# Kernel optimization log

Measured on AMD Instinct MI355X. Metric: run time of the kernel, lower is better.

## Reference

```python
import jax, jax.numpy as jnp
import numpy as np

K = 16          # self.nn_size
BALL2 = 0.2     # ball_size * 2, compared against squared L2 dists (faiss convention)

def _knn(q, db, k):
    # squared L2 pairwise distances (B,N,M) via ||q||^2 + ||db||^2 - 2 q.db
    d2 = (jnp.sum(q * q, -1)[..., None]
          + jnp.sum(db * db, -1)[..., None, :]
          - 2.0 * jnp.einsum('bnc,bmc->bnm', q, db))
    neg_d, idx = jax.lax.top_k(-d2, k)   # k smallest distances
    return -neg_d, idx                    # (B,N,K), (B,N,K)

def _cond_numbers(grouped, nball, B, N, C):
    # center by masked-ball mean, then singular values of (K,C) groups
    center = jnp.sum(grouped, axis=2, keepdims=True) / nball[..., None]
    centered = (grouped - center).reshape(-1, K, C)
    S = jnp.linalg.svd(centered, compute_uv=False)   # descending, (B*N, min(K,C))
    return (S[:, 0] / (S[:, -1] + S[:, 0])).reshape(B, N)

def setup_inputs() -> dict:
    key = jax.random.key(0)
    k1, k2 = jax.random.split(key)
    ref_points = jax.random.uniform(k1, (2, 8192, 3), dtype=jnp.float32)
    points = jax.random.uniform(k2, (2, 8192, 3), dtype=jnp.float32)
    return {"ref_points": ref_points, "points": points}

def reference(ref_points, points):
    B, N, C = ref_points.shape
    dist, idx = _knn(ref_points, ref_points, K)
    mask = dist < BALL2                                  # (B,N,K)
    nball = jnp.sum(mask.astype(ref_points.dtype), -1, keepdims=True)  # (B,N,1)

    gather = jax.vmap(lambda p, i: p[i])                 # (N,C),(N,K)->(N,K,C)
    grouped_ref = gather(ref_points, idx)                # (B,N,K,C)
    grouped_ref = jnp.where(mask[..., None], grouped_ref, 0.0)  # masked_fill_ (in-place, kept)
    ref_cond = _cond_numbers(grouped_ref, nball, B, N, C)

    grouped = gather(points, idx)                        # (B,N,K,C)
    # NOTE: original calls masked_fill (non-inplace) and DISCARDS the result -> no masking here
    cond = _cond_numbers(grouped, nball, B, N, C)

    # metric: MSE with mean reduction
    return jnp.mean((cond - ref_cond) ** 2)
```

## Files before the change

kernel.cpp:

```cpp
#include <hip/hip_runtime.h>

#define NPTS   8192
#define KNN    16
#define G      10
#define NCELLS 1000
#define CAP    32
#define CELLSZ 0.1f
#define BALL2f 0.2f
#define TRUNCM 0xFFFFE000u
#define IDXM   0x1FFFu
#define NBLK   256
#define FLTMAX 3.402823466e+38f

#define WS_ACC   0
#define WS_DONE  8
#define WS_CNT   16
#define WS_RSORT 8224
#define WS_ZERO  8216

__device__ __forceinline__ int clampg(int v) { return v < 0 ? 0 : (v > G - 1 ? G - 1 : v); }

__global__ __launch_bounds__(256) void bin_kernel(
        const float* __restrict__ ref, int* __restrict__ gcnt,
        float4* __restrict__ rs) {
    int t = blockIdx.x * 256 + threadIdx.x;
    if (t >= 2 * NPTS) return;
    int b = t >> 13, i = t & (NPTS - 1);
    const float* rb = ref + (size_t)b * NPTS * 3 + 3 * (size_t)i;
    float x = rb[0], y = rb[1], z = rb[2];
    int c = (clampg((int)(z * (float)G)) * G + clampg((int)(y * (float)G))) * G
          + clampg((int)(x * (float)G));
    int slot = atomicAdd(&gcnt[b * NCELLS + c], 1);
    if (slot < CAP)
        rs[(size_t)b * NCELLS * CAP + c * CAP + slot] =
            make_float4(x, y, z, __uint_as_float((unsigned)i));
}

__device__ __forceinline__ double cond3(double xx, double xy, double xz,
                                        double yy, double yz, double zz) {
    double q  = (xx + yy + zz) * (1.0 / 3.0);
    double a  = xx - q, b = yy - q, c = zz - q;
    double p1 = xy * xy + xz * xz + yz * yz;
    double p2 = a * a + b * b + c * c + 2.0 * p1;
    if (p2 <= 0.0) return 0.5;
    double p   = sqrt(p2 * (1.0 / 6.0));
    double inv = 1.0 / p;
    double b00 = a * inv, b11 = b * inv, b22 = c * inv;
    double b01 = xy * inv, b02 = xz * inv, b12 = yz * inv;
    double detB = b00 * (b11 * b22 - b12 * b12)
                - b01 * (b01 * b22 - b12 * b02)
                + b02 * (b01 * b12 - b11 * b02);
    double r = 0.5 * detB;
    r = fmin(1.0, fmax(-1.0, r));
    double phi = acos(r) * (1.0 / 3.0);
    double l0 = q + 2.0 * p * cos(phi);
    double l2 = q + 2.0 * p * cos(phi + 2.0943951023931953);
    double s0 = sqrt(fmax(l0, 0.0));
    double s2 = sqrt(fmax(l2, 0.0));
    return s0 / (s0 + s2);
}

__global__ __launch_bounds__(1024) void cond_knn_kernel(
        const float* __restrict__ ref, const float* __restrict__ pts,
        const float4* __restrict__ rs, const int* __restrict__ gcnt,
        double* __restrict__ acc, int* __restrict__ done,
        float* __restrict__ out) {
    __shared__ unsigned sld[8][64][17];
    __shared__ int scnt[1024];
    __shared__ int ss[1025];
    __shared__ int wsum[16];
    __shared__ unsigned cutp[64];
    __shared__ unsigned char doneA[64];
    __shared__ int flagS;

    const int tid  = threadIdx.x;
    const int w    = tid >> 6;
    const int lane = tid & 63;
    const int b     = blockIdx.x >> 7;
    const int qbase = (blockIdx.x & 127) << 6;
    const float4* rs4 = rs + (size_t)b * NCELLS * CAP;

    int myc = 0;
    if (tid < NCELLS) { myc = gcnt[b * NCELLS + tid]; myc = myc > CAP ? CAP : myc; }
    scnt[tid] = myc;
    int v = myc;
    #pragma unroll
    for (int off = 1; off < 64; off <<= 1) {
        int u = __shfl_up(v, off, 64);
        if (lane >= off) v += u;
    }
    if (lane == 63) wsum[w] = v;
    __syncthreads();
    if (tid == 0) {
        int run = 0;
        for (int i2 = 0; i2 < 16; ++i2) { int tv = wsum[i2]; wsum[i2] = run; run += tv; }
    }
    __syncthreads();
    ss[tid + 1] = v + wsum[w];
    if (tid == 0) ss[0] = 0;
    __syncthreads();

    const int spos = qbase + lane;
    int lo = 0;
    #pragma unroll
    for (int stp = 512; stp >= 1; stp >>= 1) {
        int nlo = lo + stp;
        if (ss[nlo] <= spos) lo = nlo;
    }
    const int qc = lo;
    float4 Q = rs4[qc * CAP + (spos - ss[qc])];
    const float qx = Q.x, qy = Q.y, qz = Q.z;
    const int cx = clampg((int)(qx * (float)G));
    const int cy = clampg((int)(qy * (float)G));
    const int cz = clampg((int)(qz * (float)G));

    unsigned bq[KNN];
    #pragma unroll
    for (int k = 0; k < KNN; ++k) bq[k] = 0xFFFFFFFFu;

    auto scanRange = [&](int base, int s0, int s1, unsigned cutv) {
        for (int t2 = s0; t2 < s1; ++t2) {
            float4 P = rs4[base + t2];
            float dx = qx - P.x, dy = qy - P.y, dz = qz - P.z;
            float d = fmaf(dx, dx, fmaf(dy, dy, dz * dz));
            unsigned vk = (__float_as_uint(d) & TRUNCM) | __float_as_uint(P.w);
            unsigned cv = cutv < bq[15] ? cutv : bq[15];
            if (vk < cv) {
                bq[15] = vk;
                #pragma unroll
                for (int kk = 15; kk >= 1; --kk) {
                    unsigned l2 = min(bq[kk - 1], bq[kk]);
                    unsigned h2 = max(bq[kk - 1], bq[kk]);
                    bq[kk - 1] = l2; bq[kk] = h2;
                }
            }
        }
    };

    auto mergeToW0 = [&]() {
        #pragma unroll
        for (int rnd = 0; rnd < 4; ++rnd) {
            int s = 1 << rnd;
            int slot = w >> (rnd + 1);
            __syncthreads();
            if ((w & (2 * s - 1)) == s) {
                #pragma unroll
                for (int k = 0; k < KNN; ++k) sld[slot][lane][k] = bq[k];
            }
            __syncthreads();
            if ((w & (2 * s - 1)) == 0) {
                #pragma unroll
                for (int k = 0; k < KNN; ++k) {
                    unsigned vk = sld[slot][lane][k];
                    if (vk < bq[15]) {
                        bq[15] = vk;
                        #pragma unroll
                        for (int kk = 15; kk >= 1; --kk) {
                            unsigned l2 = min(bq[kk - 1], bq[kk]);
                            unsigned h2 = max(bq[kk - 1], bq[kk]);
                            bq[kk - 1] = l2; bq[kk] = h2;
                        }
                    }
                }
            }
        }
    };

    {
        int counter = 0;
        #pragma unroll
        for (int dz = -1; dz <= 1; ++dz)
        #pragma unroll
        for (int dy = -1; dy <= 1; ++dy)
        #pragma unroll
        for (int dx = -1; dx <= 1; ++dx) {
            #pragma unroll
            for (int h = 0; h < 2; ++h) {
                int cc = counter++;
                if ((cc & 15) != w) continue;
                int nx = cx + dx, ny = cy + dy, nz = cz + dz;
                if ((unsigned)nx > (unsigned)(G - 1) || (unsigned)ny > (unsigned)(G - 1) ||
                    (unsigned)nz > (unsigned)(G - 1)) continue;
                int cell = (nz * G + ny) * G + nx;
                int cnt = scnt[cell];
                int mid = cnt >> 1;
                if (h == 0) scanRange(cell * CAP, 0, mid, 0xFFFFFFFFu);
                else        scanRange(cell * CAP, mid, cnt, 0xFFFFFFFFu);
            }
        }
    }
    mergeToW0();

    int r_done = 1;
    while (true) {
        if (tid == 0) flagS = 0;
        __syncthreads();
        if (w == 0) {
            float mx = FLTMAX;
            if (cx - r_done > 0)     mx = fminf(mx, qx - (float)(cx - r_done) * CELLSZ);
            if (cx + r_done < G - 1) mx = fminf(mx, (float)(cx + r_done + 1) * CELLSZ - qx);
            if (cy - r_done > 0)     mx = fminf(mx, qy - (float)(cy - r_done) * CELLSZ);
            if (cy + r_done < G - 1) mx = fminf(mx, (float)(cy + r_done + 1) * CELLSZ - qy);
            if (cz - r_done > 0)     mx = fminf(mx, qz - (float)(cz - r_done) * CELLSZ);
            if (cz + r_done < G - 1) mx = fminf(mx, (float)(cz + r_done + 1) * CELLSZ - qz);
            float d16t = __uint_as_float(bq[15] & TRUNCM);
            bool dn = d16t <= mx * mx * 0.998f;
            cutp[lane]  = bq[15];
            doneA[lane] = dn ? 1 : 0;
            bool anyn = __any(!dn);
            if (anyn && lane == 0) flagS = 1;
        }
        __syncthreads();
        if (!flagS || r_done >= G) break;
        int r = r_done + 1;
        if (w != 0) {
            #pragma unroll
            for (int k = 0; k < KNN; ++k) bq[k] = 0xFFFFFFFFu;
        }
        unsigned cut = cutp[lane];
        float cutub = __uint_as_float(cut | IDXM);
        bool active = !doneA[lane];
        int counter = 0;
        for (int dz = -r; dz <= r; ++dz)
        for (int dy = -r; dy <= r; ++dy)
        for (int dx = -r; dx <= r; ++dx) {
            int adx = dx < 0 ? -dx : dx, ady = dy < 0 ? -dy : dy, adz = dz < 0 ? -dz : dz;
            int m = adx > ady ? adx : ady; m = m > adz ? m : adz;
            if (m != r) continue;
            int cc = counter++;
            if ((cc & 15) != w) continue;
            if (!active) continue;
            int nx = cx + dx, ny = cy + dy, nz = cz + dz;
            if ((unsigned)nx > (unsigned)(G - 1) || (unsigned)ny > (unsigned)(G - 1) ||
                (unsigned)nz > (unsigned)(G - 1)) continue;
            float ex0 = (float)nx * CELLSZ;
            float ey0 = (float)ny * CELLSZ;
            float ez0 = (float)nz * CELLSZ;
            float ddx = fmaxf(0.f, fmaxf(ex0 - qx, qx - ex0 - CELLSZ));
            float ddy = fmaxf(0.f, fmaxf(ey0 - qy, qy - ey0 - CELLSZ));
            float ddz = fmaxf(0.f, fmaxf(ez0 - qz, qz - ez0 - CELLSZ));
            float d2min = fmaf(ddx, ddx, fmaf(ddy, ddy, ddz * ddz));
            if (d2min > cutub) continue;
            int cell = (nz * G + ny) * G + nx;
            scanRange(cell * CAP, 0, scnt[cell], cut);
        }
        mergeToW0();
        r_done = r;
    }

    if (w != 0) return;

    const float* refb = ref + (size_t)b * NPTS * 3;
    const float* ptsb = pts + (size_t)b * NPTS * 3;
    float rx[KNN], ry[KNN], rz[KNN], px[KNN], py[KNN], pz[KNN];
    int mbits = 0;
    float sRx = 0.f, sRy = 0.f, sRz = 0.f, sPx = 0.f, sPy = 0.f, sPz = 0.f;
    #pragma unroll
    for (int k = 0; k < KNN; ++k) {
        int i = (int)(bq[k] & IDXM);
        float du = __uint_as_float(bq[k] & TRUNCM);
        rx[k] = refb[3 * i]; ry[k] = refb[3 * i + 1]; rz[k] = refb[3 * i + 2];
        px[k] = ptsb[3 * i]; py[k] = ptsb[3 * i + 1]; pz[k] = ptsb[3 * i + 2];
        if (du < BALL2f) {
            mbits |= (1 << k);
            sRx += rx[k]; sRy += ry[k]; sRz += rz[k];
        }
        sPx += px[k]; sPy += py[k]; sPz += pz[k];
    }
    int nb = __popc(mbits);
    double inb = 1.0 / (double)nb;
    double cRx = (double)sRx * inb, cRy = (double)sRy * inb, cRz = (double)sRz * inb;
    double cPx = (double)sPx * inb, cPy = (double)sPy * inb, cPz = (double)sPz * inb;

    double Rxx = 0, Rxy = 0, Rxz = 0, Ryy = 0, Ryz = 0, Rzz = 0;
    double Pxx = 0, Pxy = 0, Pxz = 0, Pyy = 0, Pyz = 0, Pzz = 0;
    #pragma unroll
    for (int k = 0; k < KNN; ++k) {
        bool m = (mbits >> k) & 1;
        double ax = (m ? (double)rx[k] : 0.0) - cRx;
        double ay = (m ? (double)ry[k] : 0.0) - cRy;
        double az = (m ? (double)rz[k] : 0.0) - cRz;
        Rxx += ax * ax; Rxy += ax * ay; Rxz += ax * az;
        Ryy += ay * ay; Ryz += ay * az; Rzz += az * az;
        double bx = (double)px[k] - cPx;
        double by = (double)py[k] - cPy;
        double bz = (double)pz[k] - cPz;
        Pxx += bx * bx; Pxy += bx * by; Pxz += bx * bz;
        Pyy += by * by; Pyz += by * bz; Pzz += bz * bz;
    }
    double condR = cond3(Rxx, Rxy, Rxz, Ryy, Ryz, Rzz);
    double condP = cond3(Pxx, Pxy, Pxz, Pyy, Pyz, Pzz);
    double t = condP - condR;
    t = t * t;

    #pragma unroll
    for (int off = 32; off > 0; off >>= 1) t += __shfl_down(t, off);
    if (lane == 0) {
        atomicAdd(acc, t);
        __threadfence();
        int prev = atomicAdd(done, 1);
        if (prev == NBLK - 1) {
            __threadfence();
            double total = atomicAdd(acc, 0.0);
            out[0] = (float)(total * (1.0 / 16384.0));
        }
    }
}

extern "C" void kernel_launch(void* const* d_in, const int* in_sizes, int n_in,
                              void* d_out, int out_size, void* d_ws, size_t ws_size,
                              hipStream_t stream) {
    const float* ref = (const float*)d_in[0];
    const float* pts = (const float*)d_in[1];
    char* ws = (char*)d_ws;
    double* acc   = (double*)(ws + WS_ACC);
    int* done     = (int*)(ws + WS_DONE);
    int* gcnt     = (int*)(ws + WS_CNT);
    float4* rsort = (float4*)(ws + WS_RSORT);

    hipMemsetAsync(ws, 0, WS_ZERO, stream);
    hipLaunchKernelGGL(bin_kernel,      dim3(64),   dim3(256),  0, stream, ref, gcnt, rsort);
    hipLaunchKernelGGL(cond_knn_kernel, dim3(NBLK), dim3(1024), 0, stream,
                       ref, pts, rsort, gcnt, acc, done, (float*)d_out);
}
```

Baseline: 105.4 us.

## Fuse memset, binning and kNN into one cooperative kernel; bitonic merge

Replaces the memset, bin kernel and kNN/cond kernel with a single cooperative launch. Zeroing and binning run inside it, separated by grid-wide syncs. The change also unrolls the candidate scan by four with an early min-reject check, and replaces the per-element insertion merge across waves with a bitonic merge of two sorted 16-lists. The aim is to remove two launch and memset overheads and cut merge cost, at the price of two grid barriers and cooperative-launch constraints.

```diff
diff --git a/kernel.cpp b/kernel.cpp
--- a/kernel.cpp
+++ b/kernel.cpp
@@ -1,4 +1,7 @@
 #include <hip/hip_runtime.h>
+#include <hip/hip_cooperative_groups.h>
+
+namespace cg = cooperative_groups;
 
 #define NPTS   8192
 #define KNN    16
@@ -16,25 +19,8 @@
 #define WS_DONE  8
 #define WS_CNT   16
 #define WS_RSORT 8224
-#define WS_ZERO  8216
 
 __device__ __forceinline__ int clampg(int v) { return v < 0 ? 0 : (v > G - 1 ? G - 1 : v); }
-
-__global__ __launch_bounds__(256) void bin_kernel(
-        const float* __restrict__ ref, int* __restrict__ gcnt,
-        float4* __restrict__ rs) {
-    int t = blockIdx.x * 256 + threadIdx.x;
-    if (t >= 2 * NPTS) return;
-    int b = t >> 13, i = t & (NPTS - 1);
-    const float* rb = ref + (size_t)b * NPTS * 3 + 3 * (size_t)i;
-    float x = rb[0], y = rb[1], z = rb[2];
-    int c = (clampg((int)(z * (float)G)) * G + clampg((int)(y * (float)G))) * G
-          + clampg((int)(x * (float)G));
-    int slot = atomicAdd(&gcnt[b * NCELLS + c], 1);
-    if (slot < CAP)
-        rs[(size_t)b * NCELLS * CAP + c * CAP + slot] =
-            make_float4(x, y, z, __uint_as_float((unsigned)i));
-}
 
 __device__ __forceinline__ double cond3(double xx, double xy, double xz,
                                         double yy, double yz, double zz) {
@@ -60,9 +46,9 @@
     return s0 / (s0 + s2);
 }
 
-__global__ __launch_bounds__(1024) void cond_knn_kernel(
+__global__ __launch_bounds__(1024) void fused_kernel(
         const float* __restrict__ ref, const float* __restrict__ pts,
-        const float4* __restrict__ rs, const int* __restrict__ gcnt,
+        int* __restrict__ gcnt, float4* __restrict__ rs,
         double* __restrict__ acc, int* __restrict__ done,
         float* __restrict__ out) {
     __shared__ unsigned sld[8][64][17];
@@ -76,8 +62,34 @@
     const int tid  = threadIdx.x;
     const int w    = tid >> 6;
     const int lane = tid & 63;
-    const int b     = blockIdx.x >> 7;
-    const int qbase = (blockIdx.x & 127) << 6;
+    const int blk  = blockIdx.x;
+
+    {
+        int z = blk * 8 + tid;
+        if (tid < 8 && z < 2 * NCELLS) gcnt[z] = 0;
+        if (blk == 0 && tid == 0) { acc[0] = 0.0; done[0] = 0; }
+    }
+    __threadfence();
+    cg::this_grid().sync();
+
+    if (tid < 64) {
+        int i = blk * 64 + tid;
+        int bb = i >> 13, ii = i & (NPTS - 1);
+        const float* rb = ref + (size_t)bb * NPTS * 3 + 3 * (size_t)ii;
+        float x = rb[0], y = rb[1], z = rb[2];
+        int c = (clampg((int)(z * (float)G)) * G + clampg((int)(y * (float)G))) * G
+              + clampg((int)(x * (float)G));
+        int slot = atomicAdd(&gcnt[bb * NCELLS + c], 1);
+        if (slot < CAP)
+            rs[(size_t)bb * NCELLS * CAP + c * CAP + slot] =
+                make_float4(x, y, z, __uint_as_float((unsigned)ii));
+    }
+    __threadfence();
+    cg::this_grid().sync();
+    __threadfence();
+
+    const int b     = blk >> 7;
+    const int qbase = (blk & 127) << 6;
     const float4* rs4 = rs + (size_t)b * NCELLS * CAP;
 
     int myc = 0;
@@ -118,23 +130,71 @@
     #pragma unroll
     for (int k = 0; k < KNN; ++k) bq[k] = 0xFFFFFFFFu;
 
+    auto ins1 = [&](unsigned vk, unsigned cutv) {
+        unsigned cv = cutv < bq[15] ? cutv : bq[15];
+        if (vk < cv) {
+            bq[15] = vk;
+            #pragma unroll
+            for (int kk = 15; kk >= 1; --kk) {
+                unsigned l2 = min(bq[kk - 1], bq[kk]);
+                unsigned h2 = max(bq[kk - 1], bq[kk]);
+                bq[kk - 1] = l2; bq[kk] = h2;
+            }
+        }
+    };
+
     auto scanRange = [&](int base, int s0, int s1, unsigned cutv) {
-        for (int t2 = s0; t2 < s1; ++t2) {
+        int t2 = s0;
+        for (; t2 + 4 <= s1; t2 += 4) {
+            float4 P0 = rs4[base + t2 + 0];
+            float4 P1 = rs4[base + t2 + 1];
+            float4 P2 = rs4[base + t2 + 2];
+            float4 P3 = rs4[base + t2 + 3];
+            float dx0 = qx - P0.x, dy0 = qy - P0.y, dz0 = qz - P0.z;
+            float dx1 = qx - P1.x, dy1 = qy - P1.y, dz1 = qz - P1.z;
+            float dx2 = qx - P2.x, dy2 = qy - P2.y, dz2 = qz - P2.z;
+            float dx3 = qx - P3.x, dy3 = qy - P3.y, dz3 = qz - P3.z;
+            float d0 = fmaf(dx0, dx0, fmaf(dy0, dy0, dz0 * dz0));
+            float d1 = fmaf(dx1, dx1, fmaf(dy1, dy1, dz1 * dz1));
+            float d2 = fmaf(dx2, dx2, fmaf(dy2, dy2, dz2 * dz2));
+            float d3 = fmaf(dx3, dx3, fmaf(dy3, dy3, dz3 * dz3));
+            unsigned k0 = (__float_as_uint(d0) & TRUNCM) | __float_as_uint(P0.w);
+            unsigned k1 = (__float_as_uint(d1) & TRUNCM) | __float_as_uint(P1.w);
+            unsigned k2 = (__float_as_uint(d2) & TRUNCM) | __float_as_uint(P2.w);
+            unsigned k3 = (__float_as_uint(d3) & TRUNCM) | __float_as_uint(P3.w);
+            unsigned mn = min(min(k0, k1), min(k2, k3));
+            unsigned cv = cutv < bq[15] ? cutv : bq[15];
+            if (mn < cv) {
+                ins1(k0, cutv); ins1(k1, cutv); ins1(k2, cutv); ins1(k3, cutv);
+            }
+        }
+        for (; t2 < s1; ++t2) {
             float4 P = rs4[base + t2];
             float dx = qx - P.x, dy = qy - P.y, dz = qz - P.z;
             float d = fmaf(dx, dx, fmaf(dy, dy, dz * dz));
-            unsigned vk = (__float_as_uint(d) & TRUNCM) | __float_as_uint(P.w);
-            unsigned cv = cutv < bq[15] ? cutv : bq[15];
-            if (vk < cv) {
-                bq[15] = vk;
-                #pragma unroll
-                for (int kk = 15; kk >= 1; --kk) {
-                    unsigned l2 = min(bq[kk - 1], bq[kk]);
-                    unsigned h2 = max(bq[kk - 1], bq[kk]);
-                    bq[kk - 1] = l2; bq[kk] = h2;
+            ins1((__float_as_uint(d) & TRUNCM) | __float_as_uint(P.w), cutv);
+        }
+    };
+
+    auto bitonicMergeFromLds = [&](int slot) {
+        unsigned inc[KNN], t[KNN];
+        #pragma unroll
+        for (int k = 0; k < KNN; ++k) inc[k] = sld[slot][lane][k];
+        #pragma unroll
+        for (int i = 0; i < KNN; ++i) t[i] = min(bq[i], inc[KNN - 1 - i]);
+        #pragma unroll
+        for (int s = 8; s >= 1; s >>= 1) {
+            #pragma unroll
+            for (int i = 0; i < KNN; ++i) {
+                if ((i & s) == 0) {
+                    unsigned l2 = min(t[i], t[i | s]);
+                    unsigned h2 = max(t[i], t[i | s]);
+                    t[i] = l2; t[i | s] = h2;
                 }
             }
         }
+        #pragma unroll
+        for (int k = 0; k < KNN; ++k) bq[k] = t[k];
     };
 
     auto mergeToW0 = [&]() {
@@ -148,21 +208,7 @@
                 for (int k = 0; k < KNN; ++k) sld[slot][lane][k] = bq[k];
             }
             __syncthreads();
-            if ((w & (2 * s - 1)) == 0) {
-                #pragma unroll
-                for (int k = 0; k < KNN; ++k) {
-                    unsigned vk = sld[slot][lane][k];
-                    if (vk < bq[15]) {
-                        bq[15] = vk;
-                        #pragma unroll
-                        for (int kk = 15; kk >= 1; --kk) {
-                            unsigned l2 = min(bq[kk - 1], bq[kk]);
-                            unsigned h2 = max(bq[kk - 1], bq[kk]);
-                            bq[kk - 1] = l2; bq[kk] = h2;
-                        }
-                    }
-                }
-            }
+            if ((w & (2 * s - 1)) == 0) bitonicMergeFromLds(slot);
         }
     };
 
@@ -317,9 +363,10 @@
     int* done     = (int*)(ws + WS_DONE);
     int* gcnt     = (int*)(ws + WS_CNT);
     float4* rsort = (float4*)(ws + WS_RSORT);
-
-    hipMemsetAsync(ws, 0, WS_ZERO, stream);
-    hipLaunchKernelGGL(bin_kernel,      dim3(64),   dim3(256),  0, stream, ref, gcnt, rsort);
-    hipLaunchKernelGGL(cond_knn_kernel, dim3(NBLK), dim3(1024), 0, stream,
-                       ref, pts, rsort, gcnt, acc, done, (float*)d_out);
+    float* outp   = (float*)d_out;
+
+    void* args[] = { (void*)&ref, (void*)&pts, (void*)&gcnt, (void*)&rsort,
+                     (void*)&acc, (void*)&done, (void*)&outp };
+    hipLaunchCooperativeKernel((const void*)fused_kernel, dim3(NBLK), dim3(1024),
+                               args, 0, stream);
 }
```

New measurement: 337.1 us. 220% more time.
